# Performance work log

Hardware: AMD Instinct MI355X
Metric: run time of the kernel (lower is better)

Reference implementation:

```python
import jax, jax.numpy as jnp
import numpy as np

B, T, E, H = 8, 1024, 1024, 16
D = E // H  # per-head dim = 64


def setup_inputs() -> dict:
    key = jax.random.key(0)
    ks = jax.random.split(key, 10)
    s = 0.05
    return {
        "source": jax.random.normal(ks[0], (B, T, E), jnp.float32),
        "target": jax.random.normal(ks[1], (B, T, E), jnp.float32),
        "W_q": jax.random.normal(ks[2], (1, H, D, D), jnp.float32) * s,
        "W_v": jax.random.normal(ks[3], (1, H, D, D), jnp.float32) * s,
        "W_o": jax.random.normal(ks[4], (1, H, D, D), jnp.float32) * s,
        "W_ih": jax.random.normal(ks[5], (H, D, D), jnp.float32) * s,
        "W_hh": jax.random.normal(ks[6], (H, D, D), jnp.float32) * s,
        "b_ih": jax.random.normal(ks[7], (H, D), jnp.float32) * s,
        "b_hh": jax.random.normal(ks[8], (H, D), jnp.float32) * s,
    }


def reference(source, target, W_q, W_v, W_o, W_ih, W_hh, b_ih, b_hh):
    b, t, e = source.shape
    h = W_ih.shape[0]
    d = e // h
    # split heads: [B, H, T, d]
    q = source.reshape(b, t, h, d).transpose(0, 2, 1, 3)
    k = target.reshape(b, t, h, d).transpose(0, 2, 1, 3)
    v = k
    # per-head projections (grammar path: k is NOT projected)
    q = jnp.einsum('bhtd,hde->bhte', q, W_q[0])
    v = jnp.einsum('bhtd,hde->bhte', v, W_v[0])
    # RNN positional key generation (per head, batch_first nn.RNN, tanh).
    # step 0: input = k[:, :, 0, :], hidden = 0  ->  h1 = tanh(x @ Wih^T + b_ih + b_hh)
    k0 = k[:, :, 0, :]  # [B, H, d]
    h1 = jnp.tanh(jnp.einsum('bhd,hed->bhe', k0, W_ih) + b_ih + b_hh)
    # steps t>=1: next_word fed back as BOTH input and hidden state
    def step(hs, _):
        hn = jnp.tanh(jnp.einsum('bhd,hed->bhe', hs, W_ih) + b_ih
                      + jnp.einsum('bhd,hed->bhe', hs, W_hh) + b_hh)
        return hn, hn
    _, rest = jax.lax.scan(step, h1, None, length=t - 1)  # [T-1, B, H, d]
    nw = jnp.concatenate([h1[None], rest], axis=0).transpose(1, 2, 0, 3)  # [B,H,T,d]
    # scores / sqrt(d)  (time_attention), then merge_attn divides by sqrt(T)
    scores = jnp.einsum('bhqd,bhkd->bhqk', q, nw) / float(np.sqrt(d))
    w = jax.nn.softmax(scores / float(np.sqrt(t)), axis=-1)
    out = jnp.einsum('bhqk,bhkd->bhqd', w, v)
    out = jnp.einsum('bhtd,hde->bhte', out, W_o[0])
    return out.transpose(0, 2, 1, 3).reshape(b, t, e)
```

## Files before the change

kernel.cpp:

```cpp
#include <hip/hip_runtime.h>

typedef unsigned short u16;
typedef unsigned int   u32;
typedef short short8 __attribute__((ext_vector_type(8)));
typedef float f32x4 __attribute__((ext_vector_type(4)));
typedef _Float16 f16;
typedef f16 f16x2 __attribute__((ext_vector_type(2)));
typedef f16 f16x8 __attribute__((ext_vector_type(8)));

#define B_ 8
#define T_ 1024
#define E_ 1024
#define H_ 16
#define D_ 64
#define BH_ 128

__device__ __forceinline__ float fexp2(float x){
#if __has_builtin(__builtin_amdgcn_exp2f)
    return __builtin_amdgcn_exp2f(x);
#else
    return exp2f(x);
#endif
}

__device__ __forceinline__ float ftanh(float x){
    float xl = fminf(23.0f, fmaxf(-23.0f, x * 2.885390081777927f));
    float e2 = fexp2(xl);
    return 1.0f - 2.0f * __builtin_amdgcn_rcpf(e2 + 1.0f);
}

__device__ __forceinline__ u16 f2h(float x){
    union { f16 h; u16 u; } v; v.h = (f16)x; return v.u;
}

__device__ __forceinline__ float h2f(u16 u){
    union { u16 u; f16 h; } v; v.u = u; return (float)v.h;
}

#define DPPC(s, ctrl) ((u32)__builtin_amdgcn_update_dpp(0, (int)(s), (ctrl), 0xF, 0xF, false))

struct G8 { u32 r0, r1, r2, r3, r4, r5, r6, r7; };

__device__ __forceinline__ G8 gather16(u32 a){
    G8 g;
    u32 t = DPPC(a, 0xB1);
    g.r0 = a | (t << 16);
    g.r1 = DPPC(g.r0, 0x4E);
    g.r2 = DPPC(g.r0, 0x124);
    g.r3 = DPPC(g.r1, 0x124);
    g.r4 = DPPC(g.r0, 0x128);
    g.r5 = DPPC(g.r1, 0x128);
    g.r6 = DPPC(g.r2, 0x128);
    g.r7 = DPPC(g.r3, 0x128);
    return g;
}

__device__ __forceinline__ float fd(u32 w, u32 x, float acc){
    return __builtin_amdgcn_fdot2(__builtin_bit_cast(f16x2, w),
                                  __builtin_bit_cast(f16x2, x), acc, false);
}

__device__ __forceinline__ float perm16x(float v, bool sel){
    u32 a = __builtin_bit_cast(u32, v), b = a;
    asm volatile("v_permlane16_swap_b32 %0, %1" : "+v"(a), "+v"(b));
    return __builtin_bit_cast(float, sel ? a : b);
}
__device__ __forceinline__ float perm32x(float v, bool sel){
    u32 a = __builtin_bit_cast(u32, v), b = a;
    asm volatile("v_permlane32_swap_b32 %0, %1" : "+v"(a), "+v"(b));
    return __builtin_bit_cast(float, sel ? a : b);
}

template<bool USEPERM>
__device__ __forceinline__ u32 rnn_step(u32 hbits, const u32 (&W)[4][8], float cbias,
                                        bool q1f, bool q2f, bool sel16, bool sel32)
{
    G8 g = gather16(hbits);
    float p0 = fd(W[0][0], g.r0, 0.f);
    float p1 = fd(W[1][0], g.r0, 0.f);
    float p2 = fd(W[2][0], g.r0, 0.f);
    float p3 = fd(W[3][0], g.r0, 0.f);
    p0 = fd(W[0][1], g.r1, p0); p1 = fd(W[1][1], g.r1, p1);
    p2 = fd(W[2][1], g.r1, p2); p3 = fd(W[3][1], g.r1, p3);
    p0 = fd(W[0][2], g.r2, p0); p1 = fd(W[1][2], g.r2, p1);
    p2 = fd(W[2][2], g.r2, p2); p3 = fd(W[3][2], g.r2, p3);
    p0 = fd(W[0][3], g.r3, p0); p1 = fd(W[1][3], g.r3, p1);
    p2 = fd(W[2][3], g.r3, p2); p3 = fd(W[3][3], g.r3, p3);
    p0 = fd(W[0][4], g.r4, p0); p1 = fd(W[1][4], g.r4, p1);
    p2 = fd(W[2][4], g.r4, p2); p3 = fd(W[3][4], g.r4, p3);
    p0 = fd(W[0][5], g.r5, p0); p1 = fd(W[1][5], g.r5, p1);
    p2 = fd(W[2][5], g.r5, p2); p3 = fd(W[3][5], g.r5, p3);
    p0 = fd(W[0][6], g.r6, p0); p1 = fd(W[1][6], g.r6, p1);
    p2 = fd(W[2][6], g.r6, p2); p3 = fd(W[3][6], g.r6, p3);
    p0 = fd(W[0][7], g.r7, p0); p1 = fd(W[1][7], g.r7, p1);
    p2 = fd(W[2][7], g.r7, p2); p3 = fd(W[3][7], g.r7, p3);

    float A0 = q1f ? p1 : p0, S0 = q1f ? p0 : p1;
    float A1 = q1f ? p3 : p2, S1 = q1f ? p2 : p3;
    if (USEPERM) {
        A0 += perm16x(S0, sel16);
        A1 += perm16x(S1, sel16);
    } else {
        A0 += __shfl_xor(S0, 16);
        A1 += __shfl_xor(S1, 16);
    }
    float K  = q2f ? A1 : A0;
    float SS = q2f ? A0 : A1;
    float recv = USEPERM ? perm32x(SS, sel32) : __shfl_xor(SS, 32);
    float yv = K + recv;
    return (u32)f2h(ftanh(yv + cbias));
}

__global__ __launch_bounds__(256, 1) void proj_rnn_kernel(
    const float* __restrict__ src, const float* __restrict__ tgt,
    const float* __restrict__ Wq,  const float* __restrict__ Wv,
    const float* __restrict__ Wih, const float* __restrict__ Whh,
    const float* __restrict__ bih, const float* __restrict__ bhh,
    u16* __restrict__ qh, u16* __restrict__ vh, u16* __restrict__ nwh)
{
    int bid = blockIdx.x;
    if (bid < BH_) {
        if (threadIdx.x >= 64) return;
        __builtin_amdgcn_s_setprio(3);
        const int b = bid >> 4, h = bid & 15;
        const int l = threadIdx.x;
        const bool q1f = (l & 16) != 0;
        const bool q2f = (l & 32) != 0;

        G8 cg = gather16((u32)f2h((float)l));
        int kidx[16];
        kidx[0]  = (int)h2f((u16)(cg.r0 & 0xFFFF)); kidx[1]  = (int)h2f((u16)(cg.r0 >> 16));
        kidx[2]  = (int)h2f((u16)(cg.r1 & 0xFFFF)); kidx[3]  = (int)h2f((u16)(cg.r1 >> 16));
        kidx[4]  = (int)h2f((u16)(cg.r2 & 0xFFFF)); kidx[5]  = (int)h2f((u16)(cg.r2 >> 16));
        kidx[6]  = (int)h2f((u16)(cg.r3 & 0xFFFF)); kidx[7]  = (int)h2f((u16)(cg.r3 >> 16));
        kidx[8]  = (int)h2f((u16)(cg.r4 & 0xFFFF)); kidx[9]  = (int)h2f((u16)(cg.r4 >> 16));
        kidx[10] = (int)h2f((u16)(cg.r5 & 0xFFFF)); kidx[11] = (int)h2f((u16)(cg.r5 >> 16));
        kidx[12] = (int)h2f((u16)(cg.r6 & 0xFFFF)); kidx[13] = (int)h2f((u16)(cg.r6 >> 16));
        kidx[14] = (int)h2f((u16)(cg.r7 & 0xFFFF)); kidx[15] = (int)h2f((u16)(cg.r7 >> 16));

        u32 sx = (u32)l, sy = (u32)l;
        asm volatile("v_permlane16_swap_b32 %0, %1" : "+v"(sx), "+v"(sy));
        const bool sel16 = (sx == (u32)(l ^ 16));
        const bool ok16  = sel16 || (sy == (u32)(l ^ 16));
        u32 tx = (u32)l, ty = (u32)l;
        asm volatile("v_permlane32_swap_b32 %0, %1" : "+v"(tx), "+v"(ty));
        const bool sel32 = (tx == (u32)(l ^ 32));
        const bool ok32  = sel32 || (ty == (u32)(l ^ 32));

        const float* WI = Wih + (size_t)h * D_ * D_;
        const float* WH = Whh + (size_t)h * D_ * D_;
        float cbias = bih[h * D_ + l] + bhh[h * D_ + l];
        u32 wm[4][8], wn[4][8];
        #pragma unroll
        for (int i = 0; i < 4; ++i) {
            const float* wiR = WI + (size_t)((l & 15) + 16 * i) * D_;
            const float* whR = WH + (size_t)((l & 15) + 16 * i) * D_;
            #pragma unroll
            for (int j = 0; j < 8; ++j) {
                int k0 = kidx[2 * j], k1 = kidx[2 * j + 1];
                float wI0 = wiR[k0], wI1 = wiR[k1];
                float wH0 = whR[k0], wH1 = whR[k1];
                wn[i][j] = (u32)f2h(wI0)       | ((u32)f2h(wI1)       << 16);
                wm[i][j] = (u32)f2h(wI0 + wH0) | ((u32)f2h(wI1 + wH1) << 16);
            }
        }
        #pragma unroll
        for (int i = 0; i < 4; ++i)
            #pragma unroll
            for (int j = 0; j < 8; ++j)
                asm volatile("" : "+v"(wm[i][j]));
        asm volatile("" : "+v"(cbias));

        u16* nwp = nwh + (size_t)bid * T_ * D_;
        u32 hb = (u32)f2h(tgt[(size_t)b * T_ * E_ + h * D_ + l]);

        if (__all(ok16 && ok32)) {
            hb = rnn_step<true>(hb, wn, cbias, q1f, q2f, sel16, sel32);
            nwp[l] = (u16)hb;
            #pragma unroll 1
            for (int t = 1; t < T_; ++t) {
                hb = rnn_step<true>(hb, wm, cbias, q1f, q2f, sel16, sel32);
                nwp[(size_t)t * D_ + l] = (u16)hb;
            }
        } else {
            hb = rnn_step<false>(hb, wn, cbias, q1f, q2f, sel16, sel32);
            nwp[l] = (u16)hb;
            #pragma unroll 1
            for (int t = 1; t < T_; ++t) {
                hb = rnn_step<false>(hb, wm, cbias, q1f, q2f, sel16, sel32);
                nwp[(size_t)t * D_ + l] = (u16)hb;
            }
        }
    } else {
        int pb   = bid - BH_;
        int bh   = pb >> 5;
        int tile = pb & 31;
        int b = bh >> 4, h = bh & 15;
        int e  = threadIdx.x & 63;
        int tg = threadIdx.x >> 6;
        int t0 = tile * 32 + tg * 8;

        const float* wq = Wq + (size_t)h * D_ * D_ + e;
        const float* wv = Wv + (size_t)h * D_ * D_ + e;
        const float* s0 = src + ((size_t)b * T_ + t0) * E_ + h * D_;
        const float* g0 = tgt + ((size_t)b * T_ + t0) * E_ + h * D_;

        float aq[8] = {0,0,0,0,0,0,0,0};
        float av[8] = {0,0,0,0,0,0,0,0};
        #pragma unroll 4
        for (int d4 = 0; d4 < 16; ++d4) {
            float q0 = wq[(4*d4+0)*64], q1 = wq[(4*d4+1)*64],
                  q2 = wq[(4*d4+2)*64], q3 = wq[(4*d4+3)*64];
            float v0 = wv[(4*d4+0)*64], v1 = wv[(4*d4+1)*64],
                  v2 = wv[(4*d4+2)*64], v3 = wv[(4*d4+3)*64];
            #pragma unroll
            for (int j = 0; j < 8; ++j) {
                float4 x = *(const float4*)(s0 + (size_t)j * E_ + 4*d4);
                float4 y = *(const float4*)(g0 + (size_t)j * E_ + 4*d4);
                aq[j] += x.x*q0 + x.y*q1 + x.z*q2 + x.w*q3;
                av[j] += y.x*v0 + y.y*v1 + y.z*v2 + y.w*v3;
            }
        }
        u16* qp = qh + ((size_t)bh * T_ + t0) * D_ + e;
        #pragma unroll
        for (int j = 0; j < 8; ++j) qp[(size_t)j * D_] = f2h(aq[j] * (1.0f/256.0f));
        f16x8 vv;
        #pragma unroll
        for (int j = 0; j < 8; ++j) vv[j] = (f16)av[j];
        *(f16x8*)(vh + ((size_t)bh * D_ + e) * T_ + t0) = vv;
    }
}

#define MFMA16(a, b, c) __builtin_amdgcn_mfma_f32_16x16x32_f16(a, b, c, 0, 0, 0)

__global__ __launch_bounds__(256) void attn_kernel(
    const u16* __restrict__ qh,
    const u16* __restrict__ kh,
    const u16* __restrict__ vh,
    const float* __restrict__ Wo,
    float* __restrict__ out)
{
    __shared__ __align__(16) u16 Klds[64 * 64];
    __shared__ __align__(16) u16 Vlds[64 * 64];
    __shared__ __align__(16) u16 Plds[4][16 * 64];

    const int tid  = threadIdx.x;
    const int lane = tid & 63;
    const int w    = tid >> 6;
    const int l15  = lane & 15;
    const int quad = lane >> 4;
    const int sw   = lane & 7;
    const int bh   = blockIdx.y;
    const int qt   = blockIdx.x;

    const size_t base  = (size_t)bh * T_ * D_;
    const size_t vbase = (size_t)bh * D_ * T_;

    f16x8 aq0, aq1;
    {
        int qrow = qt * 64 + w * 16 + l15;
        const f16x8* qp = (const f16x8*)(qh + base + (size_t)qrow * 64 + quad * 8);
        aq0 = qp[0];
        aq1 = qp[4];
    }

    f32x4 oacc[4];
    #pragma unroll
    for (int i = 0; i < 4; ++i) oacc[i] = (f32x4){0.f, 0.f, 0.f, 0.f};
    float lrun[4] = {0.f, 0.f, 0.f, 0.f};

    u16* Pw = Plds[w];

    #pragma unroll 1
    for (int kt = 0; kt < 16; ++kt) {
        #pragma unroll
        for (int i = 0; i < 2; ++i) {
            int ch = tid + 256 * i;
            int r = ch >> 3, cc = ch & 7;
            short8 kval = *(const short8*)(kh + base + (size_t)(kt * 64 + r) * 64 + cc * 8);
            *(short8*)&Klds[r * 64 + ((cc ^ (r & 7)) * 8)] = kval;
            short8 vval = *(const short8*)(vh + vbase + (size_t)r * T_ + kt * 64 + cc * 8);
            *(short8*)&Vlds[r * 64 + ((cc ^ (r & 7)) * 8)] = vval;
        }
        __syncthreads();

        f32x4 sacc[4];
        #pragma unroll
        for (int u = 0; u < 4; ++u) {
            sacc[u] = (f32x4){0.f, 0.f, 0.f, 0.f};
            int row = 16 * u + l15;
            f16x8 bk0 = *(const f16x8*)&Klds[row * 64 + (((quad + 0) ^ sw) * 8)];
            f16x8 bk1 = *(const f16x8*)&Klds[row * 64 + (((quad + 4) ^ sw) * 8)];
            sacc[u] = MFMA16(aq0, bk0, sacc[u]);
            sacc[u] = MFMA16(aq1, bk1, sacc[u]);
        }

        float pr[4][4];
        #pragma unroll
        for (int r = 0; r < 4; ++r) {
            float rs = 0.f;
            #pragma unroll
            for (int u = 0; u < 4; ++u) {
                float pv = __expf(sacc[u][r]);
                pr[u][r] = pv;
                rs += pv;
            }
            #pragma unroll
            for (int off = 1; off < 16; off <<= 1)
                rs += __shfl_xor(rs, off, 16);
            lrun[r] += rs;
        }

        #pragma unroll
        for (int u = 0; u < 4; ++u) {
            int col = 16 * u + l15;
            #pragma unroll
            for (int r = 0; r < 4; ++r) {
                int row = quad * 4 + r;
                Pw[row * 64 + (((col >> 3) ^ (row & 7)) * 8) + (col & 7)] = f2h(pr[u][r]);
            }
        }

        #pragma unroll
        for (int kc = 0; kc < 2; ++kc) {
            f16x8 ap = *(const f16x8*)&Pw[l15 * 64 + (((quad + 4 * kc) ^ sw) * 8)];
            #pragma unroll
            for (int nt = 0; nt < 4; ++nt) {
                int drow = 16 * nt + l15;
                f16x8 bv = *(const f16x8*)&Vlds[drow * 64 + (((quad + 4 * kc) ^ sw) * 8)];
                oacc[nt] = MFMA16(ap, bv, oacc[nt]);
            }
        }
        __syncthreads();
    }

    const int b  = bh >> 4, hh = bh & 15;
    {
        const float* wo = Wo + (size_t)hh * D_ * D_;
        #pragma unroll
        for (int i = 0; i < 2; ++i) {
            int ch = tid + 256 * i;
            int e = ch >> 3, dc = ch & 7;
            short8 vch;
            #pragma unroll
            for (int j = 0; j < 8; ++j)
                vch[j] = (short)f2h(wo[(size_t)(dc * 8 + j) * D_ + e]);
            *(short8*)&Klds[e * 64 + ((dc ^ (e & 7)) * 8)] = vch;
        }
    }
    #pragma unroll
    for (int nt = 0; nt < 4; ++nt) {
        int col = 16 * nt + l15;
        #pragma unroll
        for (int r = 0; r < 4; ++r) {
            int row = quad * 4 + r;
            Pw[row * 64 + (((col >> 3) ^ (row & 7)) * 8) + (col & 7)] =
                f2h(oacc[nt][r] / lrun[r]);
        }
    }
    __syncthreads();

    f16x8 ao0 = *(const f16x8*)&Pw[l15 * 64 + (((quad + 0) ^ sw) * 8)];
    f16x8 ao1 = *(const f16x8*)&Pw[l15 * 64 + (((quad + 4) ^ sw) * 8)];
    f32x4 oo[4];
    #pragma unroll
    for (int nt = 0; nt < 4; ++nt) {
        oo[nt] = (f32x4){0.f, 0.f, 0.f, 0.f};
        int erow = 16 * nt + l15;
        f16x8 b0 = *(const f16x8*)&Klds[erow * 64 + (((quad + 0) ^ (erow & 7)) * 8)];
        f16x8 b1 = *(const f16x8*)&Klds[erow * 64 + (((quad + 4) ^ (erow & 7)) * 8)];
        oo[nt] = MFMA16(ao0, b0, oo[nt]);
        oo[nt] = MFMA16(ao1, b1, oo[nt]);
    }
    #pragma unroll
    for (int nt = 0; nt < 4; ++nt) {
        #pragma unroll
        for (int r = 0; r < 4; ++r) {
            int qg = qt * 64 + w * 16 + quad * 4 + r;
            int e  = 16 * nt + l15;
            out[((size_t)b * T_ + qg) * E_ + hh * D_ + e] = oo[nt][r];
        }
    }
}

extern "C" void kernel_launch(void* const* d_in, const int* in_sizes, int n_in,
                              void* d_out, int out_size, void* d_ws, size_t ws_size,
                              hipStream_t stream)
{
    const float* src = (const float*)d_in[0];
    const float* tgt = (const float*)d_in[1];
    const float* Wq  = (const float*)d_in[2];
    const float* Wv  = (const float*)d_in[3];
    const float* Wo  = (const float*)d_in[4];
    const float* Wih = (const float*)d_in[5];
    const float* Whh = (const float*)d_in[6];
    const float* bih = (const float*)d_in[7];
    const float* bhh = (const float*)d_in[8];
    float* out = (float*)d_out;

    char* ws = (char*)d_ws;
    u16* qh  = (u16*)(ws);
    u16* vh  = (u16*)(ws + (size_t)16 * 1024 * 1024);
    u16* nwh = (u16*)(ws + (size_t)32 * 1024 * 1024);

    (void)in_sizes; (void)n_in; (void)out_size; (void)ws_size;

    proj_rnn_kernel<<<dim3(BH_ + 4096), 256, 0, stream>>>(
        src, tgt, Wq, Wv, Wih, Whh, bih, bhh, qh, vh, nwh);
    attn_kernel<<<dim3(16, BH_), 256, 0, stream>>>(qh, nwh, vh, Wo, out);
}
```

Measured before the change: 413.3 us.

## Fuse RNN, projection and attention into one kernel with flag-based streaming

Merges the projection/RNN kernel and the attention kernel into a single persistent launch. RNN blocks publish each 64-step chunk of keys and bump a per-head flag, and attention blocks spin-wait on those flags so attention overlaps the serial recurrence instead of waiting for the whole RNN to finish. The RNN also carries the lane-pair packed hidden state so each step stores a 32-bit word from even lanes only. This adds a memset, spin-wait polling and a dependence on co-residency of blocks; if attention blocks occupy CUs before projection blocks finish there is a risk of stalls, bounded only by a timeout.

```diff
diff --git a/kernel.cpp b/kernel.cpp
--- a/kernel.cpp
+++ b/kernel.cpp
@@ -14,6 +14,9 @@
 #define H_ 16
 #define D_ 64
 #define BH_ 128
+#define NPROJ 4096
+#define NATTN 2048
+#define ATTN0 (BH_ + NPROJ)
 
 __device__ __forceinline__ float fexp2(float x){
 #if __has_builtin(__builtin_amdgcn_exp2f)
@@ -37,18 +40,38 @@
     union { u16 u; f16 h; } v; v.u = u; return (float)v.h;
 }
 
+__device__ __forceinline__ int ld_acq(int* p){
+    return __hip_atomic_load(p, __ATOMIC_ACQUIRE, __HIP_MEMORY_SCOPE_AGENT);
+}
+__device__ __forceinline__ int wave_wait_ge(int* p, int need, int lane){
+    int v = 0;
+    if (lane == 0) {
+        v = ld_acq(p);
+        int g = 0;
+        while (v < need) {
+            __builtin_amdgcn_s_sleep(64);
+            v = ld_acq(p);
+            if (++g > (1 << 19)) break;
+        }
+    }
+    return __builtin_amdgcn_readfirstlane(v);
+}
+
 #define DPPC(s, ctrl) ((u32)__builtin_amdgcn_update_dpp(0, (int)(s), (ctrl), 0xF, 0xF, false))
 
 struct G8 { u32 r0, r1, r2, r3, r4, r5, r6, r7; };
 
-__device__ __forceinline__ G8 gather16(u32 a){
+__device__ __forceinline__ u32 mkpair(u32 hb){
+    return hb | (DPPC(hb, 0xB1) << 16);
+}
+
+__device__ __forceinline__ G8 gather_from_pair(u32 r0){
     G8 g;
-    u32 t = DPPC(a, 0xB1);
-    g.r0 = a | (t << 16);
-    g.r1 = DPPC(g.r0, 0x4E);
-    g.r2 = DPPC(g.r0, 0x124);
+    g.r0 = r0;
+    g.r1 = DPPC(r0,   0x4E);
+    g.r2 = DPPC(r0,   0x124);
     g.r3 = DPPC(g.r1, 0x124);
-    g.r4 = DPPC(g.r0, 0x128);
+    g.r4 = DPPC(r0,   0x128);
     g.r5 = DPPC(g.r1, 0x128);
     g.r6 = DPPC(g.r2, 0x128);
     g.r7 = DPPC(g.r3, 0x128);
@@ -72,10 +95,10 @@
 }
 
 template<bool USEPERM>
-__device__ __forceinline__ u32 rnn_step(u32 hbits, const u32 (&W)[4][8], float cbias,
+__device__ __forceinline__ u32 rnn_step(u32 pair, const u32 (&W)[4][8], float cbias,
                                         bool q1f, bool q2f, bool sel16, bool sel32)
 {
-    G8 g = gather16(hbits);
+    G8 g = gather_from_pair(pair);
     float p0 = fd(W[0][0], g.r0, 0.f);
     float p1 = fd(W[1][0], g.r0, 0.f);
     float p2 = fd(W[2][0], g.r0, 0.f);
@@ -108,15 +131,19 @@
     float SS = q2f ? A0 : A1;
     float recv = USEPERM ? perm32x(SS, sel32) : __shfl_xor(SS, 32);
     float yv = K + recv;
-    return (u32)f2h(ftanh(yv + cbias));
-}
-
-__global__ __launch_bounds__(256, 1) void proj_rnn_kernel(
+    return mkpair((u32)f2h(ftanh(yv + cbias)));
+}
+
+#define MFMA16(a, b, c) __builtin_amdgcn_mfma_f32_16x16x32_f16(a, b, c, 0, 0, 0)
+
+__global__ __launch_bounds__(256, 1) void salt_fused_kernel(
     const float* __restrict__ src, const float* __restrict__ tgt,
     const float* __restrict__ Wq,  const float* __restrict__ Wv,
     const float* __restrict__ Wih, const float* __restrict__ Whh,
     const float* __restrict__ bih, const float* __restrict__ bhh,
-    u16* __restrict__ qh, u16* __restrict__ vh, u16* __restrict__ nwh)
+    const float* __restrict__ Wo,  float* __restrict__ out,
+    u16* __restrict__ qh, u16* __restrict__ vh, u16* __restrict__ nwh,
+    int* __restrict__ flags)
 {
     int bid = blockIdx.x;
     if (bid < BH_) {
@@ -127,7 +154,7 @@
         const bool q1f = (l & 16) != 0;
         const bool q2f = (l & 32) != 0;
 
-        G8 cg = gather16((u32)f2h((float)l));
+        G8 cg = gather_from_pair(mkpair((u32)f2h((float)l)));
         int kidx[16];
         kidx[0]  = (int)h2f((u16)(cg.r0 & 0xFFFF)); kidx[1]  = (int)h2f((u16)(cg.r0 >> 16));
         kidx[2]  = (int)h2f((u16)(cg.r1 & 0xFFFF)); kidx[3]  = (int)h2f((u16)(cg.r1 >> 16));
@@ -171,27 +198,51 @@
                 asm volatile("" : "+v"(wm[i][j]));
         asm volatile("" : "+v"(cbias));
 
-        u16* nwp = nwh + (size_t)bid * T_ * D_;
-        u32 hb = (u32)f2h(tgt[(size_t)b * T_ * E_ + h * D_ + l]);
+        u32* nw32 = (u32*)(nwh + (size_t)bid * T_ * D_);
+        const bool evenl = (l & 1) == 0;
+        const int  col2  = l >> 1;
+        u32 pair = mkpair((u32)f2h(tgt[(size_t)b * T_ * E_ + h * D_ + l]));
 
         if (__all(ok16 && ok32)) {
-            hb = rnn_step<true>(hb, wn, cbias, q1f, q2f, sel16, sel32);
-            nwp[l] = (u16)hb;
-            #pragma unroll 1
-            for (int t = 1; t < T_; ++t) {
-                hb = rnn_step<true>(hb, wm, cbias, q1f, q2f, sel16, sel32);
-                nwp[(size_t)t * D_ + l] = (u16)hb;
+            pair = rnn_step<true>(pair, wn, cbias, q1f, q2f, sel16, sel32);
+            if (evenl)
+                __hip_atomic_store(nw32 + col2, pair, __ATOMIC_RELAXED, __HIP_MEMORY_SCOPE_AGENT);
+            int trow = 1;
+            for (int k = 0; k < 16; ++k) {
+                const int tend = (k + 1) * 64;
+                #pragma unroll 1
+                for (; trow < tend; ++trow) {
+                    pair = rnn_step<true>(pair, wm, cbias, q1f, q2f, sel16, sel32);
+                    if (evenl)
+                        __hip_atomic_store(nw32 + trow * 32 + col2, pair,
+                                           __ATOMIC_RELAXED, __HIP_MEMORY_SCOPE_AGENT);
+                }
+                asm volatile("s_waitcnt vmcnt(0)" ::: "memory");
+                if (l == 0)
+                    __hip_atomic_store(&flags[bid], k + 1,
+                                       __ATOMIC_RELAXED, __HIP_MEMORY_SCOPE_AGENT);
             }
         } else {
-            hb = rnn_step<false>(hb, wn, cbias, q1f, q2f, sel16, sel32);
-            nwp[l] = (u16)hb;
-            #pragma unroll 1
-            for (int t = 1; t < T_; ++t) {
-                hb = rnn_step<false>(hb, wm, cbias, q1f, q2f, sel16, sel32);
-                nwp[(size_t)t * D_ + l] = (u16)hb;
-            }
-        }
-    } else {
+            pair = rnn_step<false>(pair, wn, cbias, q1f, q2f, sel16, sel32);
+            if (evenl)
+                __hip_atomic_store(nw32 + col2, pair, __ATOMIC_RELAXED, __HIP_MEMORY_SCOPE_AGENT);
+            int trow = 1;
+            for (int k = 0; k < 16; ++k) {
+                const int tend = (k + 1) * 64;
+                #pragma unroll 1
+                for (; trow < tend; ++trow) {
+                    pair = rnn_step<false>(pair, wm, cbias, q1f, q2f, sel16, sel32);
+                    if (evenl)
+                        __hip_atomic_store(nw32 + trow * 32 + col2, pair,
+                                           __ATOMIC_RELAXED, __HIP_MEMORY_SCOPE_AGENT);
+                }
+                asm volatile("s_waitcnt vmcnt(0)" ::: "memory");
+                if (l == 0)
+                    __hip_atomic_store(&flags[bid], k + 1,
+                                       __ATOMIC_RELAXED, __HIP_MEMORY_SCOPE_AGENT);
+            }
+        }
+    } else if (bid < ATTN0) {
         int pb   = bid - BH_;
         int bh   = pb >> 5;
         int tile = pb & 31;
@@ -228,157 +279,159 @@
         #pragma unroll
         for (int j = 0; j < 8; ++j) vv[j] = (f16)av[j];
         *(f16x8*)(vh + ((size_t)bh * D_ + e) * T_ + t0) = vv;
-    }
-}
-
-#define MFMA16(a, b, c) __builtin_amdgcn_mfma_f32_16x16x32_f16(a, b, c, 0, 0, 0)
-
-__global__ __launch_bounds__(256) void attn_kernel(
-    const u16* __restrict__ qh,
-    const u16* __restrict__ kh,
-    const u16* __restrict__ vh,
-    const float* __restrict__ Wo,
-    float* __restrict__ out)
-{
-    __shared__ __align__(16) u16 Klds[64 * 64];
-    __shared__ __align__(16) u16 Vlds[64 * 64];
-    __shared__ __align__(16) u16 Plds[4][16 * 64];
-
-    const int tid  = threadIdx.x;
-    const int lane = tid & 63;
-    const int w    = tid >> 6;
-    const int l15  = lane & 15;
-    const int quad = lane >> 4;
-    const int sw   = lane & 7;
-    const int bh   = blockIdx.y;
-    const int qt   = blockIdx.x;
-
-    const size_t base  = (size_t)bh * T_ * D_;
-    const size_t vbase = (size_t)bh * D_ * T_;
-
-    f16x8 aq0, aq1;
-    {
-        int qrow = qt * 64 + w * 16 + l15;
-        const f16x8* qp = (const f16x8*)(qh + base + (size_t)qrow * 64 + quad * 8);
-        aq0 = qp[0];
-        aq1 = qp[4];
-    }
-
-    f32x4 oacc[4];
-    #pragma unroll
-    for (int i = 0; i < 4; ++i) oacc[i] = (f32x4){0.f, 0.f, 0.f, 0.f};
-    float lrun[4] = {0.f, 0.f, 0.f, 0.f};
-
-    u16* Pw = Plds[w];
-
-    #pragma unroll 1
-    for (int kt = 0; kt < 16; ++kt) {
-        #pragma unroll
-        for (int i = 0; i < 2; ++i) {
-            int ch = tid + 256 * i;
-            int r = ch >> 3, cc = ch & 7;
-            short8 kval = *(const short8*)(kh + base + (size_t)(kt * 64 + r) * 64 + cc * 8);
-            *(short8*)&Klds[r * 64 + ((cc ^ (r & 7)) * 8)] = kval;
-            short8 vval = *(const short8*)(vh + vbase + (size_t)r * T_ + kt * 64 + cc * 8);
-            *(short8*)&Vlds[r * 64 + ((cc ^ (r & 7)) * 8)] = vval;
-        }
+
         __syncthreads();
-
-        f32x4 sacc[4];
-        #pragma unroll
-        for (int u = 0; u < 4; ++u) {
-            sacc[u] = (f32x4){0.f, 0.f, 0.f, 0.f};
-            int row = 16 * u + l15;
-            f16x8 bk0 = *(const f16x8*)&Klds[row * 64 + (((quad + 0) ^ sw) * 8)];
-            f16x8 bk1 = *(const f16x8*)&Klds[row * 64 + (((quad + 4) ^ sw) * 8)];
-            sacc[u] = MFMA16(aq0, bk0, sacc[u]);
-            sacc[u] = MFMA16(aq1, bk1, sacc[u]);
-        }
-
-        float pr[4][4];
-        #pragma unroll
-        for (int r = 0; r < 4; ++r) {
-            float rs = 0.f;
+        if (threadIdx.x == 0)
+            __hip_atomic_fetch_add(&flags[BH_], 1,
+                                   __ATOMIC_RELEASE, __HIP_MEMORY_SCOPE_AGENT);
+    } else {
+        __shared__ __align__(16) u16 Klds[64 * 64];
+        __shared__ __align__(16) u16 Vlds[64 * 64];
+        __shared__ __align__(16) u16 Plds[4][16 * 64];
+
+        const int ab   = bid - ATTN0;
+        const int tid  = threadIdx.x;
+        const int lane = tid & 63;
+        const int w    = tid >> 6;
+        const int l15  = lane & 15;
+        const int quad = lane >> 4;
+        const int sw   = lane & 7;
+        const int bh   = ab >> 4;
+        const int qt   = ab & 15;
+
+        const size_t base  = (size_t)bh * T_ * D_;
+        const size_t vbase = (size_t)bh * D_ * T_;
+
+        wave_wait_ge(&flags[BH_], NPROJ, lane);
+
+        f16x8 aq0, aq1;
+        {
+            int qrow = qt * 64 + w * 16 + l15;
+            const f16x8* qp = (const f16x8*)(qh + base + (size_t)qrow * 64 + quad * 8);
+            aq0 = qp[0];
+            aq1 = qp[4];
+        }
+
+        f32x4 oacc[4];
+        #pragma unroll
+        for (int i = 0; i < 4; ++i) oacc[i] = (f32x4){0.f, 0.f, 0.f, 0.f};
+        float lrun[4] = {0.f, 0.f, 0.f, 0.f};
+
+        u16* Pw = Plds[w];
+        int seen = 0;
+
+        #pragma unroll 1
+        for (int kt = 0; kt < 16; ++kt) {
+            if (seen < kt + 1)
+                seen = wave_wait_ge(&flags[bh], kt + 1, lane);
+
+            #pragma unroll
+            for (int i = 0; i < 2; ++i) {
+                int ch = tid + 256 * i;
+                int r = ch >> 3, cc = ch & 7;
+                short8 kval = *(const short8*)(nwh + base + (size_t)(kt * 64 + r) * 64 + cc * 8);
+                *(short8*)&Klds[r * 64 + ((cc ^ (r & 7)) * 8)] = kval;
+                short8 vval = *(const short8*)(vh + vbase + (size_t)r * T_ + kt * 64 + cc * 8);
+                *(short8*)&Vlds[r * 64 + ((cc ^ (r & 7)) * 8)] = vval;
+            }
+            __syncthreads();
+
+            f32x4 sacc[4];
             #pragma unroll
             for (int u = 0; u < 4; ++u) {
-                float pv = __expf(sacc[u][r]);
-                pr[u][r] = pv;
-                rs += pv;
-            }
-            #pragma unroll
-            for (int off = 1; off < 16; off <<= 1)
-                rs += __shfl_xor(rs, off, 16);
-            lrun[r] += rs;
-        }
-
-        #pragma unroll
-        for (int u = 0; u < 4; ++u) {
-            int col = 16 * u + l15;
+                sacc[u] = (f32x4){0.f, 0.f, 0.f, 0.f};
+                int row = 16 * u + l15;
+                f16x8 bk0 = *(const f16x8*)&Klds[row * 64 + (((quad + 0) ^ sw) * 8)];
+                f16x8 bk1 = *(const f16x8*)&Klds[row * 64 + (((quad + 4) ^ sw) * 8)];
+                sacc[u] = MFMA16(aq0, bk0, sacc[u]);
+                sacc[u] = MFMA16(aq1, bk1, sacc[u]);
+            }
+
+            float pr[4][4];
+            #pragma unroll
+            for (int r = 0; r < 4; ++r) {
+                float rs = 0.f;
+                #pragma unroll
+                for (int u = 0; u < 4; ++u) {
+                    float pv = __expf(sacc[u][r]);
+                    pr[u][r] = pv;
+                    rs += pv;
+                }
+                #pragma unroll
+                for (int off = 1; off < 16; off <<= 1)
+                    rs += __shfl_xor(rs, off, 16);
+                lrun[r] += rs;
+            }
+
+            #pragma unroll
+            for (int u = 0; u < 4; ++u) {
+                int col = 16 * u + l15;
+                #pragma unroll
+                for (int r = 0; r < 4; ++r) {
+                    int row = quad * 4 + r;
+                    Pw[row * 64 + (((col >> 3) ^ (row & 7)) * 8) + (col & 7)] = f2h(pr[u][r]);
+                }
+            }
+
+            #pragma unroll
+            for (int kc = 0; kc < 2; ++kc) {
+                f16x8 ap = *(const f16x8*)&Pw[l15 * 64 + (((quad + 4 * kc) ^ sw) * 8)];
+                #pragma unroll
+                for (int nt = 0; nt < 4; ++nt) {
+                    int drow = 16 * nt + l15;
+                    f16x8 bv = *(const f16x8*)&Vlds[drow * 64 + (((quad + 4 * kc) ^ sw) * 8)];
+                    oacc[nt] = MFMA16(ap, bv, oacc[nt]);
+                }
+            }
+            __syncthreads();
+        }
+
+        const int b  = bh >> 4, hh = bh & 15;
+        {
+            const float* wo = Wo + (size_t)hh * D_ * D_;
+            #pragma unroll
+            for (int i = 0; i < 2; ++i) {
+                int ch = tid + 256 * i;
+                int e = ch >> 3, dc = ch & 7;
+                short8 vch;
+                #pragma unroll
+                for (int j = 0; j < 8; ++j)
+                    vch[j] = (short)f2h(wo[(size_t)(dc * 8 + j) * D_ + e]);
+                *(short8*)&Klds[e * 64 + ((dc ^ (e & 7)) * 8)] = vch;
+            }
+        }
+        #pragma unroll
+        for (int nt = 0; nt < 4; ++nt) {
+            int col = 16 * nt + l15;
             #pragma unroll
             for (int r = 0; r < 4; ++r) {
                 int row = quad * 4 + r;
-                Pw[row * 64 + (((col >> 3) ^ (row & 7)) * 8) + (col & 7)] = f2h(pr[u][r]);
-            }
-        }
-
-        #pragma unroll
-        for (int kc = 0; kc < 2; ++kc) {
-            f16x8 ap = *(const f16x8*)&Pw[l15 * 64 + (((quad + 4 * kc) ^ sw) * 8)];
-            #pragma unroll
-            for (int nt = 0; nt < 4; ++nt) {
-                int drow = 16 * nt + l15;
-                f16x8 bv = *(const f16x8*)&Vlds[drow * 64 + (((quad + 4 * kc) ^ sw) * 8)];
-                oacc[nt] = MFMA16(ap, bv, oacc[nt]);
+                Pw[row * 64 + (((col >> 3) ^ (row & 7)) * 8) + (col & 7)] =
+                    f2h(oacc[nt][r] / lrun[r]);
             }
         }
         __syncthreads();
-    }
-
-    const int b  = bh >> 4, hh = bh & 15;
-    {
-        const float* wo = Wo + (size_t)hh * D_ * D_;
-        #pragma unroll
-        for (int i = 0; i < 2; ++i) {
-            int ch = tid + 256 * i;
-            int e = ch >> 3, dc = ch & 7;
-            short8 vch;
-            #pragma unroll
-            for (int j = 0; j < 8; ++j)
-                vch[j] = (short)f2h(wo[(size_t)(dc * 8 + j) * D_ + e]);
-            *(short8*)&Klds[e * 64 + ((dc ^ (e & 7)) * 8)] = vch;
-        }
-    }
-    #pragma unroll
-    for (int nt = 0; nt < 4; ++nt) {
-        int col = 16 * nt + l15;
-        #pragma unroll
-        for (int r = 0; r < 4; ++r) {
-            int row = quad * 4 + r;
-            Pw[row * 64 + (((col >> 3) ^ (row & 7)) * 8) + (col & 7)] =
-                f2h(oacc[nt][r] / lrun[r]);
-        }
-    }
-    __syncthreads();
-
-    f16x8 ao0 = *(const f16x8*)&Pw[l15 * 64 + (((quad + 0) ^ sw) * 8)];
-    f16x8 ao1 = *(const f16x8*)&Pw[l15 * 64 + (((quad + 4) ^ sw) * 8)];
-    f32x4 oo[4];
-    #pragma unroll
-    for (int nt = 0; nt < 4; ++nt) {
-        oo[nt] = (f32x4){0.f, 0.f, 0.f, 0.f};
-        int erow = 16 * nt + l15;
-        f16x8 b0 = *(const f16x8*)&Klds[erow * 64 + (((quad + 0) ^ (erow & 7)) * 8)];
-        f16x8 b1 = *(const f16x8*)&Klds[erow * 64 + (((quad + 4) ^ (erow & 7)) * 8)];
-        oo[nt] = MFMA16(ao0, b0, oo[nt]);
-        oo[nt] = MFMA16(ao1, b1, oo[nt]);
-    }
-    #pragma unroll
-    for (int nt = 0; nt < 4; ++nt) {
-        #pragma unroll
-        for (int r = 0; r < 4; ++r) {
-            int qg = qt * 64 + w * 16 + quad * 4 + r;
-            int e  = 16 * nt + l15;
-            out[((size_t)b * T_ + qg) * E_ + hh * D_ + e] = oo[nt][r];
+
+        f16x8 ao0 = *(const f16x8*)&Pw[l15 * 64 + (((quad + 0) ^ sw) * 8)];
+        f16x8 ao1 = *(const f16x8*)&Pw[l15 * 64 + (((quad + 4) ^ sw) * 8)];
+        f32x4 oo[4];
+        #pragma unroll
+        for (int nt = 0; nt < 4; ++nt) {
+            oo[nt] = (f32x4){0.f, 0.f, 0.f, 0.f};
+            int erow = 16 * nt + l15;
+            f16x8 b0 = *(const f16x8*)&Klds[erow * 64 + (((quad + 0) ^ (erow & 7)) * 8)];
+            f16x8 b1 = *(const f16x8*)&Klds[erow * 64 + (((quad + 4) ^ (erow & 7)) * 8)];
+            oo[nt] = MFMA16(ao0, b0, oo[nt]);
+            oo[nt] = MFMA16(ao1, b1, oo[nt]);
+        }
+        #pragma unroll
+        for (int nt = 0; nt < 4; ++nt) {
+            #pragma unroll
+            for (int r = 0; r < 4; ++r) {
+                int qg = qt * 64 + w * 16 + quad * 4 + r;
+                int e  = 16 * nt + l15;
+                out[((size_t)b * T_ + qg) * E_ + hh * D_ + e] = oo[nt][r];
+            }
         }
     }
 }
@@ -402,10 +455,11 @@
     u16* qh  = (u16*)(ws);
     u16* vh  = (u16*)(ws + (size_t)16 * 1024 * 1024);
     u16* nwh = (u16*)(ws + (size_t)32 * 1024 * 1024);
+    int* flags = (int*)(ws + (size_t)48 * 1024 * 1024);
 
     (void)in_sizes; (void)n_in; (void)out_size; (void)ws_size;
 
-    proj_rnn_kernel<<<dim3(BH_ + 4096), 256, 0, stream>>>(
-        src, tgt, Wq, Wv, Wih, Whh, bih, bhh, qh, vh, nwh);
-    attn_kernel<<<dim3(16, BH_), 256, 0, stream>>>(qh, nwh, vh, Wo, out);
-}
+    hipMemsetAsync(flags, 0, 4096, stream);
+    salt_fused_kernel<<<dim3(BH_ + NPROJ + NATTN), 256, 0, stream>>>(
+        src, tgt, Wq, Wv, Wih, Whh, bih, bhh, Wo, out, qh, vh, nwh, flags);
+}
```

Measured after the change: 719.7 us. 74.1% more time.
